# Kernel optimization log

Measured on AMD Instinct MI355X. Metric: run time of the kernel, lower is better.

The kernel has to match this reference:

```python
import jax, jax.numpy as jnp
import numpy as np

D_MODEL = 512
N_HEADS = 8
D_K = D_MODEL // N_HEADS
MAX_LEN = 512  # max_seq_len; rel table has 2*MAX_LEN-1 rows


def setup_inputs() -> dict:
    key = jax.random.key(0)
    ks = jax.random.split(key, 7)
    B, S = 8, 512
    s = 1.0 / np.sqrt(D_MODEL)
    return {
        "x": jax.random.normal(ks[0], (B, S, D_MODEL), jnp.float32),
        "Wq": jax.random.normal(ks[1], (D_MODEL, D_MODEL), jnp.float32) * s,
        "bq": jnp.zeros((D_MODEL,), jnp.float32),
        "Wk": jax.random.normal(ks[2], (D_MODEL, D_MODEL), jnp.float32) * s,
        "bk": jnp.zeros((D_MODEL,), jnp.float32),
        "Wv": jax.random.normal(ks[3], (D_MODEL, D_MODEL), jnp.float32) * s,
        "bv": jnp.zeros((D_MODEL,), jnp.float32),
        "Wo": jax.random.normal(ks[4], (D_MODEL, D_MODEL), jnp.float32) * s,
        "bo": jnp.zeros((D_MODEL,), jnp.float32),
        "rel_embed": jax.random.normal(ks[5], (2 * MAX_LEN - 1, D_MODEL), jnp.float32) * 0.02,
    }


def reference(x, Wq, bq, Wk, bk, Wv, bv, Wo, bo, rel_embed):
    B, S, _ = x.shape
    scale = np.sqrt(D_K).astype(np.float32)

    def split_heads(t):  # (B,S,D) -> (B,H,S,dk)
        return t.reshape(B, S, N_HEADS, D_K).transpose(0, 2, 1, 3)

    q = split_heads(x @ Wq.T + bq)
    k = split_heads(x @ Wk.T + bk)
    v = split_heads(x @ Wv.T + bv)

    scores = jnp.einsum('bhqd,bhkd->bhqk', q, k) / scale

    # relative position bias: idx[q_pos, k_pos] = k_pos - q_pos + MAX_LEN - 1
    pos = jnp.arange(S)
    rel_idx = pos[None, :] - pos[:, None] + (MAX_LEN - 1)  # (S,S)
    rel_bias = rel_embed[rel_idx].reshape(S, S, N_HEADS, D_K)  # (S,S,H,dk)
    scores = scores + jnp.einsum('bhqd,qkhd->bhqk', q, rel_bias)

    attn = jax.nn.softmax(scores, axis=-1)
    out = jnp.einsum('bhqk,bhkd->bhqd', attn, v)  # (B,H,S,dk)
    out = out.transpose(0, 2, 1, 3).reshape(B, S, D_MODEL)
    return out @ Wo.T + bo
```

## Files before the change

### kernel.cpp

```cpp
#include <hip/hip_runtime.h>
#include <math.h>

#define B_  8
#define S_  512
#define D_  512
#define H_  8
#define DK_ 64

typedef __attribute__((ext_vector_type(8))) short short8;
typedef __attribute__((ext_vector_type(4))) float f32x4;

#define MFMA_BF16(a, b, c) __builtin_amdgcn_mfma_f32_16x16x32_bf16(a, b, c, 0, 0, 0)

__device__ __forceinline__ unsigned bf16_rne(float x) {
    unsigned u = __float_as_uint(x);
    return (u + 0x7FFFu + ((u >> 16) & 1u)) >> 16;
}
__device__ __forceinline__ float bf16f(unsigned h) { return __uint_as_float(h << 16); }

__device__ __forceinline__ void glds16(const ushort* g, ushort* l) {
    __builtin_amdgcn_global_load_lds(
        (const __attribute__((address_space(1))) unsigned int*)g,
        (__attribute__((address_space(3))) unsigned int*)l,
        16, 0, 0);
}

__global__ __launch_bounds__(256)
void conv_pl(const float* __restrict__ x,
             const float* __restrict__ wq, const float* __restrict__ wk,
             const float* __restrict__ wv, const float* __restrict__ wo,
             const float* __restrict__ rel,
             ushort* __restrict__ Xh, ushort* __restrict__ Xl,
             ushort* __restrict__ Wqh, ushort* __restrict__ Wql,
             ushort* __restrict__ Wkh, ushort* __restrict__ Wkl,
             ushort* __restrict__ Wvh, ushort* __restrict__ Wvl,
             ushort* __restrict__ Woh, ushort* __restrict__ Wol,
             ushort* __restrict__ Rg) {
    const int bid = blockIdx.x;
    if (bid >= 3072) {
        const int idx = (bid - 3072) * 256 + threadIdx.x;
        const int d2 = idx & 31;
        const int rr = (idx >> 5) % 1152;
        const int h  = idx / (1152 * 32);
        unsigned v0 = 0, v1 = 0;
        if (rr >= 64 && rr < 64 + 1023) {
            const float* s = &rel[(size_t)(rr - 64) * 512 + h * 64 + d2 * 2];
            v0 = bf16_rne(s[0]); v1 = bf16_rne(s[1]);
        }
        *(uint*)&Rg[((size_t)h * 1152 + rr) * 64 + d2 * 2] = v0 | (v1 << 16);
        return;
    }
    const float* src; ushort* dh; ushort* dl; int i4;
    if (bid < 2048) {
        src = x; dh = Xh; dl = Xl; i4 = bid * 256 + threadIdx.x;
    } else {
        const int r = bid - 2048;
        const int wsel = r >> 8;
        src = (wsel == 0) ? wq : (wsel == 1) ? wk : (wsel == 2) ? wv : wo;
        dh  = (wsel == 0) ? Wqh : (wsel == 1) ? Wkh : (wsel == 2) ? Wvh : Woh;
        dl  = (wsel == 0) ? Wql : (wsel == 1) ? Wkl : (wsel == 2) ? Wvl : Wol;
        i4 = (r & 255) * 256 + threadIdx.x;
    }
    const float4 v = ((const float4*)src)[i4];
    unsigned h[4], l[4];
    const float* vp = &v.x;
    #pragma unroll
    for (int j = 0; j < 4; ++j) { h[j] = bf16_rne(vp[j]); l[j] = bf16_rne(vp[j] - bf16f(h[j])); }
    ((uint2*)dh)[i4] = make_uint2(h[0] | (h[1] << 16), h[2] | (h[3] << 16));
    ((uint2*)dl)[i4] = make_uint2(l[0] | (l[1] << 16), l[2] | (l[3] << 16));
}

template<int XB, int OM>
__global__ __launch_bounds__(256, 3)
void gemm_mfma(const ushort* __restrict__ Xhp, const ushort* __restrict__ Xlp,
               const ushort* __restrict__ Yh0, const ushort* __restrict__ Yl0,
               const ushort* __restrict__ Yh1, const ushort* __restrict__ Yl1,
               const float* __restrict__ bias0, const float* __restrict__ bias1,
               float scale0, float scale1,
               float* __restrict__ outF,
               ushort* __restrict__ oh0, ushort* __restrict__ ol0,
               ushort* __restrict__ oh1, ushort* __restrict__ ol1) {
    __shared__ ushort Xs[2][2][64 * 64];
    __shared__ ushort Ys[2][64 * 64];

    const int z = blockIdx.z;
    const ushort* Yhp = z ? Yh1 : Yh0;
    const float*  bias = z ? bias1 : bias0;
    const float   scale = z ? scale1 : scale0;
    ushort* ohp = z ? oh1 : oh0;
    ushort* olp = z ? ol1 : ol0;

    const int tid = threadIdx.x;
    const int w = tid >> 6, lane = tid & 63;
    const int g = lane >> 4, c = lane & 15;
    const int rloc = lane >> 3, cc8 = lane & 7;
    const int cp = cc8 ^ rloc;
    const int r0 = blockIdx.y * 64;
    const int c0 = blockIdx.x * 64;

    const f32x4 fz = {0.f, 0.f, 0.f, 0.f};
    f32x4 acc[2][2] = {{fz, fz}, {fz, fz}};

    auto stage = [&](int kt, int buf) {
        const int k0 = kt * 64;
        #pragma unroll
        for (int j = 0; j < 6; ++j) {
            const int seg = w * 6 + j;
            const int p = seg >> 3;
            const int rgrp = seg & 7;
            const int row = rgrp * 8 + rloc;
            const ushort* gb;
            if (p == 2) {
                gb = Yhp + (size_t)(c0 + row) * 512 + k0 + cp * 8;
            } else {
                const ushort* Xp = p ? Xlp : Xhp;
                if (XB == 0) {
                    gb = Xp + (size_t)(r0 + row) * 512 + k0 + cp * 8;
                } else {
                    const int b = r0 >> 9, s0 = r0 & 511, hh = k0 >> 6;
                    gb = Xp + (((size_t)(b * 8 + hh)) * 512 + s0 + row) * 64 + cp * 8;
                }
            }
            ushort* lb = (p == 2) ? &Ys[buf][0] : &Xs[buf][p][0];
            glds16(gb, lb + rgrp * 512);
        }
    };

    auto compute = [&](int buf) {
        #pragma unroll
        for (int ks = 0; ks < 2; ++ks) {
            short8 axh[2], axl[2], byh[2];
            const int wm = (w >> 1) * 32, wn = (w & 1) * 32;
            #pragma unroll
            for (int t = 0; t < 2; ++t) {
                int row = wm + t * 16 + c;
                int off = row * 64 + (((ks * 4 + g) ^ (row & 7)) * 8);
                axh[t] = *(const short8*)&Xs[buf][0][off];
                axl[t] = *(const short8*)&Xs[buf][1][off];
                row = wn + t * 16 + c;
                off = row * 64 + (((ks * 4 + g) ^ (row & 7)) * 8);
                byh[t] = *(const short8*)&Ys[buf][off];
            }
            #pragma unroll
            for (int tm = 0; tm < 2; ++tm)
                #pragma unroll
                for (int tn = 0; tn < 2; ++tn) {
                    acc[tm][tn] = MFMA_BF16(axh[tm], byh[tn], acc[tm][tn]);
                    acc[tm][tn] = MFMA_BF16(axl[tm], byh[tn], acc[tm][tn]);
                }
        }
    };

    stage(0, 0);
    __syncthreads();
    for (int kt = 0; kt < 8; ++kt) {
        if (kt < 7) stage(kt + 1, (kt + 1) & 1);
        compute(kt & 1);
        __syncthreads();
    }

    const int wm = (w >> 1) * 32, wn = (w & 1) * 32;
    if (OM == 0) {
        #pragma unroll
        for (int tn = 0; tn < 2; ++tn) {
            const int gc = c0 + wn + tn * 16 + c;
            const float bv = bias[gc];
            #pragma unroll
            for (int tm = 0; tm < 2; ++tm)
                #pragma unroll
                for (int i = 0; i < 4; ++i) {
                    const int gr = r0 + wm + tm * 16 + g * 4 + i;
                    outF[(size_t)gr * 512 + gc] = acc[tm][tn][i] + bv;
                }
        }
    } else if (OM == 2) {
        #pragma unroll
        for (int tn = 0; tn < 2; ++tn) {
            const int gc = c0 + wn + tn * 16 + c;
            const int h = gc >> 6, dk = gc & 63;
            const float bv = bias[gc];
            #pragma unroll
            for (int tm = 0; tm < 2; ++tm)
                #pragma unroll
                for (int i = 0; i < 4; ++i) {
                    const int gr = r0 + wm + tm * 16 + g * 4 + i;
                    const int b = gr >> 9, s = gr & 511;
                    const float v = (acc[tm][tn][i] + bv) * scale;
                    const unsigned hb = bf16_rne(v);
                    const size_t a = (((size_t)(b * 8 + h)) * 512 + s) * 64 + dk;
                    ohp[a] = (ushort)hb;
                    if (olp) olp[a] = (ushort)bf16_rne(v - bf16f(hb));
                }
        }
    } else {
        #pragma unroll
        for (int tm = 0; tm < 2; ++tm)
            #pragma unroll
            for (int i = 0; i < 4; ++i) {
                const int gr = r0 + wm + tm * 16 + g * 4 + i;
                const int h = gr >> 6, dk = gr & 63;
                const float bv = bias[gr];
                #pragma unroll
                for (int tn = 0; tn < 2; ++tn) {
                    const int gc = c0 + wn + tn * 16 + c;
                    const int b = gc >> 9, s = gc & 511;
                    const float v = acc[tm][tn][i] + bv;
                    const size_t a = (((size_t)(b * 8 + h)) * 64 + dk) * 512 + s;
                    ohp[a] = (ushort)bf16_rne(v);
                }
            }
    }
}

__global__ __launch_bounds__(512, 2)
void attn_mfma8(const ushort* __restrict__ Qhp, const ushort* __restrict__ Qlp,
                const ushort* __restrict__ Khp, const ushort* __restrict__ Vhp,
                const ushort* __restrict__ Rg,
                ushort* __restrict__ Oh, ushort* __restrict__ Ol) {
    __shared__ ushort Ksm[2][64 * 64];
    __shared__ ushort Vsm[2][64 * 64];
    __shared__ ushort Rsm[2][128 * 64];

    const int tid  = threadIdx.x;
    const int w    = tid >> 6;
    const int half = w >> 2;
    const int wl   = w & 3;
    const int tidh = tid & 255;
    const int lane = tid & 63;
    const int g    = lane >> 4;
    const int c    = lane & 15;
    const int rloc = lane >> 3, cc8 = lane & 7;
    const int bh   = blockIdx.y;
    const int h    = bh & 7;
    const int qwb  = blockIdx.x * 64;
    const int qw   = qwb + wl * 16;

    ushort* Usm = &Rsm[half][wl * 1376];

    const ushort* KhB = Khp + (size_t)bh * 512 * 64;
    const ushort* VhB = Vhp + (size_t)bh * 64 * 512;
    const ushort* RgH = Rg + (size_t)h * 1152 * 64;

    uint4 rv[4];
    auto issue_rel = [&](int kt) {
        const int rbase = kt * 64 - qwb + 512;
        #pragma unroll
        for (int j = 0; j < 4; ++j) {
            const int cd = j * 256 + tidh, row = cd >> 3, cc = cd & 7;
            rv[j] = *(const uint4*)&RgH[(size_t)(rbase + row) * 64 + cc * 8];
        }
    };

    issue_rel(half * 4);
    short8 qfh[2], qfl[2];
    #pragma unroll
    for (int ks = 0; ks < 2; ++ks) {
        const size_t qi = ((size_t)bh * 512 + qw + c) * 64 + ks * 32 + g * 8;
        qfh[ks] = *(const short8*)&Qhp[qi];
        qfl[ks] = *(const short8*)&Qlp[qi];
    }

    const f32x4 fz = {0.f, 0.f, 0.f, 0.f};
    f32x4 o[4] = {fz, fz, fz, fz};
    float m = -INFINITY, l = 0.f;

    for (int t = 0; t < 4; ++t) {
        const int kt = half * 4 + t;
        const int k0 = kt * 64;
        __syncthreads();

        #pragma unroll
        for (int j = 0; j < 4; ++j) {
            const int cd = j * 256 + tidh, row = cd >> 3, cc = cd & 7;
            *(uint4*)&Rsm[half][row * 64 + ((cc ^ (row & 7)) << 3)] = rv[j];
        }
        if (wl < 2) {
            ushort* lb = &Ksm[half][wl * 32 * 64];
            #pragma unroll
            for (int j = 0; j < 4; ++j) {
                const int row = wl * 32 + j * 8 + rloc;
                const int tcq = row >> 4, cq = row & 15;
                const int key = ((tcq & 1) << 5) + ((cq >> 2) << 3)
                              + ((tcq >> 1) << 2) + (cq & 3);
                glds16(KhB + (size_t)(k0 + key) * 64 + ((cc8 ^ rloc) << 3),
                       lb + j * 512);
            }
        } else {
            const ushort* gb = VhB + k0 + (size_t)(wl - 2) * 32 * 512;
            ushort* lb = &Vsm[half][(wl - 2) * 32 * 64];
            #pragma unroll
            for (int j = 0; j < 4; ++j)
                glds16(gb + (size_t)(j * 8 + rloc) * 512 + ((cc8 ^ rloc) << 3),
                       lb + j * 512);
        }

        if (t + 1 < 4) {
            issue_rel(kt + 1);
            asm volatile("s_waitcnt vmcnt(4) lgkmcnt(0)" ::: "memory");
        } else {
            asm volatile("s_waitcnt vmcnt(0) lgkmcnt(0)" ::: "memory");
        }
        __builtin_amdgcn_s_barrier();

        f32x4 u[5];
        #pragma unroll
        for (int ut = 0; ut < 5; ++ut) u[ut] = fz;
        #pragma unroll
        for (int ks = 0; ks < 2; ++ks)
            #pragma unroll
            for (int ut = 0; ut < 5; ++ut) {
                const int rl = 48 - 16 * wl + c + ut * 16;
                const short8 rf = *(const short8*)
                    &Rsm[half][rl * 64 + (((ks * 4 + g) ^ (c & 7)) << 3)];
                u[ut] = MFMA_BF16(qfh[ks], rf, u[ut]);
            }

        f32x4 st[4];
        #pragma unroll
        for (int tc = 0; tc < 4; ++tc) st[tc] = fz;
        #pragma unroll
        for (int ks = 0; ks < 2; ++ks)
            #pragma unroll
            for (int tc = 0; tc < 4; ++tc) {
                const int row = tc * 16 + c;
                const int chv = ((ks * 4 + g) ^ (row & 7)) * 8;
                const short8 kh8 = *(const short8*)&Ksm[half][row * 64 + chv];
                st[tc] = MFMA_BF16(kh8, qfh[ks], st[tc]);
                st[tc] = MFMA_BF16(kh8, qfl[ks], st[tc]);
            }

        __syncthreads();

        #pragma unroll
        for (int ut = 0; ut < 5; ++ut)
            #pragma unroll
            for (int i = 0; i < 4; ++i)
                Usm[(g * 4 + i) * 86 + c + ut * 16] = (ushort)bf16_rne(u[ut][i]);

        asm volatile("s_waitcnt lgkmcnt(0)" ::: "memory");

        #pragma unroll
        for (int tc = 0; tc < 4; ++tc)
            #pragma unroll
            for (int i = 0; i < 4; ++i) {
                const int key = ((tc & 1) << 5) + 8 * g + ((tc >> 1) << 2) + i;
                st[tc][i] += bf16f(Usm[c * 85 + key + 15]);
            }

        float tm = fmaxf(fmaxf(st[0][0], st[0][1]), fmaxf(st[0][2], st[0][3]));
        #pragma unroll
        for (int tc = 1; tc < 4; ++tc) {
            const float t2 = fmaxf(fmaxf(st[tc][0], st[tc][1]),
                                   fmaxf(st[tc][2], st[tc][3]));
            tm = fmaxf(tm, t2);
        }
        tm = fmaxf(tm, __shfl_xor(tm, 16));
        tm = fmaxf(tm, __shfl_xor(tm, 32));
        const float mn = fmaxf(m, tm);
        const float corr = __expf(m - mn);
        m = mn;
        l *= corr;
        #pragma unroll
        for (int dt = 0; dt < 4; ++dt) o[dt] *= corr;

        uint pk[4][2];
        #pragma unroll
        for (int tc = 0; tc < 4; ++tc) {
            const float p0 = __expf(st[tc][0] - mn);
            const float p1 = __expf(st[tc][1] - mn);
            const float p2 = __expf(st[tc][2] - mn);
            const float p3 = __expf(st[tc][3] - mn);
            l += (p0 + p1) + (p2 + p3);
            pk[tc][0] = bf16_rne(p0) | (bf16_rne(p1) << 16);
            pk[tc][1] = bf16_rne(p2) | (bf16_rne(p3) << 16);
        }

        #pragma unroll
        for (int ks = 0; ks < 2; ++ks) {
            union { uint u4[4]; short8 s8; } pb;
            pb.u4[0] = pk[ks][0];
            pb.u4[1] = pk[ks][1];
            pb.u4[2] = pk[ks + 2][0];
            pb.u4[3] = pk[ks + 2][1];
            #pragma unroll
            for (int dt = 0; dt < 4; ++dt) {
                const int row = dt * 16 + c;
                const int chv = ((ks * 4 + g) ^ (row & 7)) * 8;
                const short8 vh8 = *(const short8*)&Vsm[half][row * 64 + chv];
                o[dt] = MFMA_BF16(vh8, pb.s8, o[dt]);
            }
        }
    }

    float lt = l;
    lt += __shfl_xor(lt, 16);
    lt += __shfl_xor(lt, 32);

    __syncthreads();

    float* Ob = (float*)&Rsm[half][0];
    const int qcol = wl * 16 + c;
    #pragma unroll
    for (int dt = 0; dt < 4; ++dt)
        #pragma unroll
        for (int i = 0; i < 4; ++i)
            Ob[(dt * 16 + g * 4 + i) * 64 + qcol] = o[dt][i];
    float2* MlB = (float2*)&Ksm[0][0];
    if (lane < 16) MlB[half * 64 + qcol] = make_float2(m, lt);
    __syncthreads();

    const int q   = tid >> 3;
    const int dk0 = (tid & 7) * 8;
    const float2 a = MlB[q], b2 = MlB[64 + q];
    const float mm = fmaxf(a.x, b2.x);
    float w0 = __expf(a.x - mm), w1 = __expf(b2.x - mm);
    const float inv = 1.0f / (a.y * w0 + b2.y * w1);
    w0 *= inv; w1 *= inv;
    const float* O0 = (const float*)&Rsm[0][0];
    const float* O1 = (const float*)&Rsm[1][0];
    unsigned hb[8], lb8[8];
    #pragma unroll
    for (int e = 0; e < 8; ++e) {
        const int d = dk0 + e;
        const float v = O0[d * 64 + q] * w0 + O1[d * 64 + q] * w1;
        hb[e] = bf16_rne(v);
        lb8[e] = bf16_rne(v - bf16f(hb[e]));
    }
    const size_t ob = ((size_t)bh * 512 + qwb + q) * 64 + dk0;
    *(uint4*)&Oh[ob] = make_uint4(hb[0] | (hb[1] << 16), hb[2] | (hb[3] << 16),
                                  hb[4] | (hb[5] << 16), hb[6] | (hb[7] << 16));
    *(uint4*)&Ol[ob] = make_uint4(lb8[0] | (lb8[1] << 16), lb8[2] | (lb8[3] << 16),
                                  lb8[4] | (lb8[5] << 16), lb8[6] | (lb8[7] << 16));
}

extern "C" void kernel_launch(void* const* d_in, const int* in_sizes, int n_in,
                              void* d_out, int out_size, void* d_ws, size_t ws_size,
                              hipStream_t stream) {
    const float* x   = (const float*)d_in[0];
    const float* Wq  = (const float*)d_in[1];
    const float* bq  = (const float*)d_in[2];
    const float* Wk  = (const float*)d_in[3];
    const float* bk  = (const float*)d_in[4];
    const float* Wv  = (const float*)d_in[5];
    const float* bv  = (const float*)d_in[6];
    const float* Wo  = (const float*)d_in[7];
    const float* bo  = (const float*)d_in[8];
    const float* rel = (const float*)d_in[9];
    float* out = (float*)d_out;

    const size_t NP = (size_t)B_ * H_ * S_ * DK_;
    const size_t WP = (size_t)D_ * D_;
    ushort* Xh  = (ushort*)d_ws;
    ushort* Xl  = Xh + NP;
    ushort* Wqh = Xl + NP;
    ushort* Wql = Wqh + WP;
    ushort* Wkh = Wql + WP;
    ushort* Wkl = Wkh + WP;
    ushort* Wvh = Wkl + WP;
    ushort* Wvl = Wvh + WP;
    ushort* Woh = Wvl + WP;
    ushort* Wol = Woh + WP;
    ushort* Qh  = Wol + WP;
    ushort* Ql  = Qh + NP;
    ushort* Kh  = Ql + NP;
    ushort* Kl  = Kh + NP;
    ushort* Vh  = Kl + NP;
    ushort* Rg  = Vh + NP;
    ushort* Oh  = Rg + 589824;
    ushort* Ol  = Oh + NP;

    conv_pl<<<4224, 256, 0, stream>>>(x, Wq, Wk, Wv, Wo, rel,
                                      Xh, Xl, Wqh, Wql, Wkh, Wkl, Wvh, Wvl, Woh, Wol, Rg);

    gemm_mfma<0, 2><<<dim3(8, 64, 2), 256, 0, stream>>>(
        Xh, Xl, Wqh, Wql, Wkh, Wkl, bq, bk, 1.0f, 0.125f,
        nullptr, Qh, Ql, Kh, nullptr);
    gemm_mfma<0, 3><<<dim3(64, 8, 1), 256, 0, stream>>>(
        Wvh, Wvl, Xh, Xl, nullptr, nullptr, bv, nullptr, 1.0f, 1.0f,
        nullptr, Vh, nullptr, nullptr, nullptr);

    attn_mfma8<<<dim3(8, 64), 512, 0, stream>>>(
        Qh, Ql, Kh, Vh, Rg, Oh, Ol);

    gemm_mfma<1, 0><<<dim3(8, 64, 1), 256, 0, stream>>>(
        Oh, Ol, Woh, Wol, nullptr, nullptr, bo, nullptr, 1.0f, 1.0f,
        out, nullptr, nullptr, nullptr, nullptr);
}
```

Baseline: 90.24 us.

## Tune waits, priorities and LDS layouts in projection and attention kernels

In the GEMM kernel, the full __syncthreads pairs are replaced with explicit vmcnt waits plus raw s_barrier, so later prefetched stages need not be drained. In the attention kernel, s_setprio brackets the MFMA sections, the relative-bias scratch in LDS gets a new padded stride with vectorized uint2 reads in place of scalar ushort loads, and the output staging buffer uses a rotated column index to avoid bank conflicts. Each of these trims LDS or synchronization stalls. The vmcnt(6) count must match the number of loads stage issues, or correctness breaks.

```diff
diff --git a/kernel.cpp b/kernel.cpp
--- a/kernel.cpp
+++ b/kernel.cpp
@@ -152,11 +152,16 @@
     };
 
     stage(0, 0);
-    __syncthreads();
     for (int kt = 0; kt < 8; ++kt) {
-        if (kt < 7) stage(kt + 1, (kt + 1) & 1);
+        if (kt < 7) {
+            stage(kt + 1, (kt + 1) & 1);
+            asm volatile("s_waitcnt vmcnt(6)" ::: "memory");
+        } else {
+            asm volatile("s_waitcnt vmcnt(0)" ::: "memory");
+        }
+        __builtin_amdgcn_s_barrier();
         compute(kt & 1);
-        __syncthreads();
+        __builtin_amdgcn_s_barrier();
     }
 
     const int wm = (w >> 1) * 32, wn = (w & 1) * 32;
@@ -235,7 +240,7 @@
     const int qwb  = blockIdx.x * 64;
     const int qw   = qwb + wl * 16;
 
-    ushort* Usm = &Rsm[half][wl * 1376];
+    ushort* Usm = &Rsm[half][wl * 1424];
 
     const ushort* KhB = Khp + (size_t)bh * 512 * 64;
     const ushort* VhB = Vhp + (size_t)bh * 64 * 512;
@@ -302,6 +307,7 @@
         }
         __builtin_amdgcn_s_barrier();
 
+        __builtin_amdgcn_s_setprio(1);
         f32x4 u[5];
         #pragma unroll
         for (int ut = 0; ut < 5; ++ut) u[ut] = fz;
@@ -328,6 +334,7 @@
                 st[tc] = MFMA_BF16(kh8, qfh[ks], st[tc]);
                 st[tc] = MFMA_BF16(kh8, qfl[ks], st[tc]);
             }
+        __builtin_amdgcn_s_setprio(0);
 
         __syncthreads();
 
@@ -335,17 +342,19 @@
         for (int ut = 0; ut < 5; ++ut)
             #pragma unroll
             for (int i = 0; i < 4; ++i)
-                Usm[(g * 4 + i) * 86 + c + ut * 16] = (ushort)bf16_rne(u[ut][i]);
+                Usm[(g * 4 + i) * 89 + c + ut * 16 + 1] = (ushort)bf16_rne(u[ut][i]);
 
         asm volatile("s_waitcnt lgkmcnt(0)" ::: "memory");
 
         #pragma unroll
-        for (int tc = 0; tc < 4; ++tc)
-            #pragma unroll
-            for (int i = 0; i < 4; ++i) {
-                const int key = ((tc & 1) << 5) + 8 * g + ((tc >> 1) << 2) + i;
-                st[tc][i] += bf16f(Usm[c * 85 + key + 15]);
-            }
+        for (int tc = 0; tc < 4; ++tc) {
+            const int key0 = ((tc & 1) << 5) + 8 * g + ((tc >> 1) << 2);
+            const uint2 uv = *(const uint2*)&Usm[88 * c + key0 + 16];
+            st[tc][0] += bf16f(uv.x & 0xffffu);
+            st[tc][1] += bf16f(uv.x >> 16);
+            st[tc][2] += bf16f(uv.y & 0xffffu);
+            st[tc][3] += bf16f(uv.y >> 16);
+        }
 
         float tm = fmaxf(fmaxf(st[0][0], st[0][1]), fmaxf(st[0][2], st[0][3]));
         #pragma unroll
@@ -375,6 +384,7 @@
             pk[tc][1] = bf16_rne(p2) | (bf16_rne(p3) << 16);
         }
 
+        __builtin_amdgcn_s_setprio(1);
         #pragma unroll
         for (int ks = 0; ks < 2; ++ks) {
             union { uint u4[4]; short8 s8; } pb;
@@ -390,6 +400,7 @@
                 o[dt] = MFMA_BF16(vh8, pb.s8, o[dt]);
             }
         }
+        __builtin_amdgcn_s_setprio(0);
     }
 
     float lt = l;
@@ -403,8 +414,10 @@
     #pragma unroll
     for (int dt = 0; dt < 4; ++dt)
         #pragma unroll
-        for (int i = 0; i < 4; ++i)
-            Ob[(dt * 16 + g * 4 + i) * 64 + qcol] = o[dt][i];
+        for (int i = 0; i < 4; ++i) {
+            const int row = dt * 16 + g * 4 + i;
+            Ob[row * 64 + ((qcol + row) & 63)] = o[dt][i];
+        }
     float2* MlB = (float2*)&Ksm[0][0];
     if (lane < 16) MlB[half * 64 + qcol] = make_float2(m, lt);
     __syncthreads();
@@ -422,7 +435,8 @@
     #pragma unroll
     for (int e = 0; e < 8; ++e) {
         const int d = dk0 + e;
-        const float v = O0[d * 64 + q] * w0 + O1[d * 64 + q] * w1;
+        const int colr = (q + d) & 63;
+        const float v = O0[d * 64 + colr] * w0 + O1[d * 64 + colr] * w1;
         hb[e] = bf16_rne(v);
         lb8[e] = bf16_rne(v - bf16f(hb[e]));
     }
```

Result: no change. 88.87 us (-1.5%).
